# Optimization experiments

Hardware: AMD Instinct MI355X
Metric: run time of the kernel (lower is better)

The kernel has to match this reference:

```python
import jax, jax.numpy as jnp
import numpy as np

H = 128
V = 50000
B = 128
T_C = 50
T_I = 32
T_Q = 32
EPISODES = 3


def gru_cell(x, h, Wih, Whh, bih, bhh):
    # torch GRUCell math
    gi = x @ Wih.T + bih
    gh = h @ Whh.T + bhh
    ir, iz, inn = jnp.split(gi, 3, axis=-1)
    hr, hz, hn = jnp.split(gh, 3, axis=-1)
    r = jax.nn.sigmoid(ir + hr)
    z = jax.nn.sigmoid(iz + hz)
    n = jnp.tanh(inn + r * hn)
    return (1.0 - z) * n + z * h


def gru_outputs(x, Wih, Whh, bih, bhh):
    # x: (N, T, H) -> hidden at every step, (N, T, H)
    h0 = jnp.zeros((x.shape[0], x.shape[2]), x.dtype)
    def step(h, xt):
        h2 = gru_cell(xt, h, Wih, Whh, bih, bhh)
        return h2, h2
    _, ys = jax.lax.scan(step, h0, jnp.swapaxes(x, 0, 1))
    return jnp.swapaxes(ys, 0, 1)


def setup_inputs():
    key = jax.random.key(0)
    ks = iter(jax.random.split(key, 48))
    s = 0.05
    def mat(shape):
        return (jax.random.normal(next(ks), shape) * s).astype(jnp.float32)
    def gru_p(in_dim):
        return mat((3 * H, in_dim)), mat((3 * H, H)), mat((3 * H,)), mat((3 * H,))
    embed = mat((V, H)).at[0].set(0.0)  # padding_idx=0
    ig_Wih, ig_Whh, ig_bih, ig_bhh = gru_p(H)
    qg_Wih, qg_Whh, qg_bih, qg_bhh = gru_p(H)
    at_Wih, at_Whh, at_bih, at_bhh = gru_p(H)
    me_Wih, me_Whh, me_bih, me_bhh = gru_p(H)
    an_Wih, an_Whh, an_bih, an_bhh = gru_p(2 * H)
    gate_W1 = mat((H, 4 * H)); gate_b1 = mat((H,))
    gate_W2 = mat((1, H)); gate_b2 = mat((1,))
    fc_W = mat((V, H)); fc_b = jnp.zeros((V,), jnp.float32)
    facts = jax.random.randint(next(ks), (B, T_C, T_I), 0, V)
    fact_masks = jnp.zeros((B, T_C, T_I), jnp.int32)  # 0 == real token
    questions = jax.random.randint(next(ks), (B, T_Q), 0, V)
    question_masks = jnp.zeros((B, T_Q), jnp.int32)
    return dict(facts=facts, fact_masks=fact_masks, questions=questions,
                question_masks=question_masks, num_decode=8, embed=embed,
                ig_Wih=ig_Wih, ig_Whh=ig_Whh, ig_bih=ig_bih, ig_bhh=ig_bhh,
                qg_Wih=qg_Wih, qg_Whh=qg_Whh, qg_bih=qg_bih, qg_bhh=qg_bhh,
                at_Wih=at_Wih, at_Whh=at_Whh, at_bih=at_bih, at_bhh=at_bhh,
                me_Wih=me_Wih, me_Whh=me_Whh, me_bih=me_bih, me_bhh=me_bhh,
                an_Wih=an_Wih, an_Whh=an_Whh, an_bih=an_bih, an_bhh=an_bhh,
                gate_W1=gate_W1, gate_b1=gate_b1, gate_W2=gate_W2, gate_b2=gate_b2,
                fc_W=fc_W, fc_b=fc_b)


def reference(facts, fact_masks, questions, question_masks, num_decode, embed,
              ig_Wih, ig_Whh, ig_bih, ig_bhh,
              qg_Wih, qg_Whh, qg_bih, qg_bhh,
              at_Wih, at_Whh, at_bih, at_bhh,
              me_Wih, me_Whh, me_bih, me_bhh,
              an_Wih, an_Whh, an_bih, an_bhh,
              gate_W1, gate_b1, gate_W2, gate_b2, fc_W, fc_b):
    Bv, Tc, Ti = facts.shape
    Hd = embed.shape[1]

    # ---- fact encoding: one batched GRU over all B*T_C facts ----
    f = facts.reshape(Bv * Tc, Ti)
    emb = embed[f]                                            # (B*Tc, Ti, H)
    outs = gru_outputs(emb, ig_Wih, ig_Whh, ig_bih, ig_bhh)
    flen = jnp.sum(fact_masks.reshape(Bv * Tc, Ti) == 0, axis=-1)
    enc_f = jnp.take_along_axis(outs, (flen - 1)[:, None, None], axis=1)[:, 0]
    enc_f = enc_f.reshape(Bv, Tc, Hd)                         # (B, T_C, H)

    # ---- question encoding ----
    qouts = gru_outputs(embed[questions], qg_Wih, qg_Whh, qg_bih, qg_bhh)
    qlen = jnp.sum(question_masks == 0, axis=-1)
    q = jnp.take_along_axis(qouts, (qlen - 1)[:, None, None], axis=1)[:, 0]  # (B, H)

    # ---- episodic memory ----
    memory = q
    facts_t = jnp.swapaxes(enc_f, 0, 1)                       # (T_C, B, H)
    for _ in range(EPISODES):
        m = memory
        def ep_step(h, ft):
            z = jnp.concatenate([ft * q, ft * m, jnp.abs(ft - q), jnp.abs(ft - m)], axis=-1)
            g = jax.nn.sigmoid(jnp.tanh(z @ gate_W1.T + gate_b1) @ gate_W2.T + gate_b2)  # (B,1)
            h2 = gru_cell(ft, h, at_Wih, at_Whh, at_bih, at_bhh)
            return g * h2 + (1.0 - g) * h, None
        e, _ = jax.lax.scan(ep_step, jnp.zeros_like(memory), facts_t)
        memory = gru_cell(e, memory, me_Wih, me_Whh, me_bih, me_bhh)

    # ---- answer decoding (y_{t-1} stays the <s> embedding, as in the source) ----
    y0 = jnp.broadcast_to(embed[2], (Bv, Hd))                 # <s> token id = 2
    yq = jnp.concatenate([y0, q], axis=-1)                    # (B, 2H)
    def dec_step(h, _):
        h2 = gru_cell(yq, h, an_Wih, an_Whh, an_bih, an_bhh)
        return h2, jax.nn.log_softmax(h2 @ fc_W.T + fc_b, axis=-1)
    _, dec = jax.lax.scan(dec_step, memory, None, length=num_decode)  # (T, B, V)
    return jnp.swapaxes(dec, 0, 1).reshape(Bv * num_decode, -1)
```

## Files before the change

kernel.cpp:

```cpp
#include <hip/hip_runtime.h>
#include <math.h>

#define H   128
#define H3  384
#define TC  50
#define TI  32
#define TQ  32
#define NB  128
#define NF  (NB*TC)
#define EPISODES 3
#define LSLICE 25

typedef short  bf16x8 __attribute__((ext_vector_type(8)));
typedef short  bf16x4 __attribute__((ext_vector_type(4)));
typedef float  f32x4  __attribute__((ext_vector_type(4)));

__device__ __forceinline__ float dot4(float4 a, float4 b) {
  return a.x*b.x + a.y*b.y + a.z*b.z + a.w*b.w;
}
__device__ __forceinline__ float sigm(float x) { return 1.f/(1.f + __expf(-x)); }
__device__ __forceinline__ float tanh_f(float x) { return 1.f - 2.f/(1.f + __expf(2.f*x)); }
__device__ __forceinline__ float gru_comb(float ir, float iz, float inn,
                                          float hr, float hz, float hn, float h) {
  float r = sigm(ir + hr);
  float z = sigm(iz + hz);
  float n = tanh_f(inn + r*hn);
  return (1.f - z)*n + z*h;
}
__device__ __forceinline__ short f2bf(float x) {
  union { float f; unsigned u; } v; v.f = x;
  unsigned r = v.u + 0x7fffu + ((v.u >> 16) & 1u);
  return (short)(r >> 16);
}
__device__ __forceinline__ float bf2f(short s) {
  union { unsigned u; float f; } v; v.u = ((unsigned)(unsigned short)s) << 16;
  return v.f;
}
__device__ __forceinline__ bf16x8 pack8(float4 lo, float4 hi) {
  bf16x8 o;
  o[0]=f2bf(lo.x); o[1]=f2bf(lo.y); o[2]=f2bf(lo.z); o[3]=f2bf(lo.w);
  o[4]=f2bf(hi.x); o[5]=f2bf(hi.y); o[6]=f2bf(hi.z); o[7]=f2bf(hi.w);
  return o;
}

// ... 68 lines not shown
  int q = lane >> 4, l15 = lane & 15;
  f32x4 acc[8];
  #pragma unroll
  for (int nt = 0; nt < 8; ++nt) { acc[nt][0]=0.f; acc[nt][1]=0.f; acc[nt][2]=0.f; acc[nt][3]=0.f; }
  int mrow = wave*16 + l15;
  #pragma unroll
  for (int kf = 0; kf < 4; ++kf) {
    bf16x8 a = *(bf16x8*)&As[mrow][q*8 + kf*32];
    #pragma unroll
    for (int nt = 0; nt < 8; ++nt) {
      bf16x8 b = *(bf16x8*)&Bs[nt*16 + l15][q*8 + kf*32];
      acc[nt] = __builtin_amdgcn_mfma_f32_16x16x32_bf16(a, b, acc[nt], 0, 0, 0);
    }
  }
  __syncthreads();
  #pragma unroll
  for (int nt = 0; nt < 8; ++nt) {
    int col = nt*16 + l15;
    float bv = bias[bn*128 + col];
    #pragma unroll
    for (int reg = 0; reg < 4; ++reg)
      Bs[wave*16 + q*4 + reg][col] = f2bf(acc[nt][reg] + bv);
  }
  __syncthreads();
  #pragma unroll
  for (int i = 0; i < 4; ++i) {
    int idx = tid + i*256;
    int r = idx >> 4, e = (idx & 15)*8;
    int gr = bm*64 + r;
    if (gr < M) *(bf16x8*)(C + (size_t)gr*N + bn*128 + e) = *(bf16x8*)&Bs[r][e];
  }
}

__global__ __launch_bounds__(256) void k_copy(const float* __restrict__ src,
    float* __restrict__ dst, int n)
{
  int i = blockIdx.x*256 + threadIdx.x;
  if (i < n) dst[i] = src[i];
}

#define GI_STR 392
__global__ __launch_bounds__(512) void k_recgru2(
    const short* __restrict__ GI, const int* __restrict__ toks,
    const int* __restrict__ masks,
    const float* __restrict__ Whh, const float* __restrict__ bhh,
    float* __restrict__ enc_out, int steps)
{
  __shared__ __align__(16) short hsb[2][16][136];
  __shared__ __align__(16) short gib[2][16][GI_STR];
  __shared__ int ltoks[16*TI];
  __shared__ int enc_step_s[16];
  int tid = threadIdx.x;
  int lane = tid & 63, wave = tid >> 6;
  int q = lane >> 4, l15 = lane & 15;
  int seq0 = blockIdx.x * 16;

  for (int i = tid; i < 2*16*136; i += 512) ((short*)hsb)[i] = 0;
  if (toks) for (int i = tid; i < 16*steps; i += 512)
    ltoks[i] = toks[(size_t)seq0*steps + i];
  if (tid < 16) {
    int fl = 0;
    for (int i = 0; i < steps; ++i) fl += (masks[(size_t)(seq0+tid)*steps + i] == 0);
    int et = fl - 1; if (et < 0) et = 0; if (et >= steps) et = steps-1;
    enc_step_s[tid] = et;
  }
  bf16x8 wfrag[3][4];
  #pragma unroll
  for (int i = 0; i < 3; ++i) {
    int n = 16*wave + 128*i + l15;
    const float* wr = Whh + (size_t)n*H + q*8;
    #pragma unroll
    for (int kf = 0; kf < 4; ++kf)
      wfrag[i][kf] = pack8(*(const float4*)(wr + kf*32), *(const float4*)(wr + kf*32 + 4));
  }
  int c = 16*wave + l15;
  float bh0 = bhh[c], bh1 = bhh[c+H], bh2 = bhh[c+2*H];
  int ch0 = tid, ch1 = tid + 512;
  int r0 = ch0/48, o0 = ch0 - r0*48;
  int r1 = ch1/48, o1 = ch1 - r1*48;
  __syncthreads();
  int es[4];
  #pragma unroll
  for (int reg = 0; reg < 4; ++reg) es[reg] = enc_step_s[q*4 + reg];

  {
    size_t row0 = toks ? (size_t)ltoks[r0*steps] : ((size_t)(seq0 + r0)*steps);
    *(bf16x8*)&gib[0][r0][o0*8] = *((const bf16x8*)(GI + row0*H3) + o0);
    if (tid < 256) {
      size_t row1 = toks ? (size_t)ltoks[r1*steps] : ((size_t)(seq0 + r1)*steps);
      *(bf16x8*)&gib[0][r1][o1*8] = *((const bf16x8*)(GI + row1*H3) + o1);
    }
  }
  __syncthreads();

  float hreg[4] = {0.f, 0.f, 0.f, 0.f};
  for (int t = 0; t < steps; ++t) {
    bf16x8 pf0, pf1;
    bool havepf = (t + 1 < steps);
    if (havepf) {
      size_t row0 = toks ? (size_t)ltoks[r0*steps + t + 1]
                         : ((size_t)(seq0 + r0)*steps + t + 1);
      pf0 = *((const bf16x8*)(GI + row0*H3) + o0);
      if (tid < 256) {
        size_t row1 = toks ? (size_t)ltoks[r1*steps + t + 1]
                           : ((size_t)(seq0 + r1)*steps + t + 1);
        pf1 = *((const bf16x8*)(GI + row1*H3) + o1);
      }
    }
    f32x4 acc[3];
    #pragma unroll
    for (int i = 0; i < 3; ++i) { acc[i][0]=0.f; acc[i][1]=0.f; acc[i][2]=0.f; acc[i][3]=0.f; }
    #pragma unroll
    for (int kf = 0; kf < 4; ++kf) {
      bf16x8 a = *(bf16x8*)&hsb[t & 1][l15][kf*32 + q*8];
      #pragma unroll
      for (int i = 0; i < 3; ++i)
        acc[i] = __builtin_amdgcn_mfma_f32_16x16x32_bf16(a, wfrag[i][kf], acc[i], 0, 0, 0);
    }
    #pragma unroll
    for (int reg = 0; reg < 4; ++reg) {
      int row = q*4 + reg;
      float gr = bf2f(gib[t & 1][row][c]);
      float gz = bf2f(gib[t & 1][row][c + 128]);
      float gn = bf2f(gib[t & 1][row][c + 256]);
      float hnew = gru_comb(gr, gz, gn,
                            acc[0][reg] + bh0, acc[1][reg] + bh1, acc[2][reg] + bh2,
                            hreg[reg]);
      hreg[reg] = hnew;
      hsb[(t + 1) & 1][row][c] = f2bf(hnew);
      if (t == es[reg]) enc_out[(size_t)(seq0 + row)*H + c] = hnew;
    }
    if (havepf) {
      *(bf16x8*)&gib[(t + 1) & 1][r0][o0*8] = pf0;
      if (tid < 256) *(bf16x8*)&gib[(t + 1) & 1][r1][o1*8] = pf1;
    }
    __syncthreads();
  }
}

__global__ __launch_bounds__(512) void k_recgru3(
    const short* __restrict__ GI, const int* __restrict__ toks,
    const int* __restrict__ masks,
    const float* __restrict__ Whh, const float* __restrict__ bhh,
    float* __restrict__ enc_out, int steps)
{
  __shared__ __align__(16) short hsb[2][32][136];
  __shared__ __align__(16) short gib[2][25][GI_STR];
  __shared__ int ltoks[25*TI];
  __shared__ int enc_step_s[25];
  int tid = threadIdx.x;
  int lane = tid & 63, wave = tid >> 6;
  int q = lane >> 4, l15 = lane & 15;
  int seq0 = blockIdx.x * 25;

  for (int i = tid; i < 2*32*136; i += 512) ((short*)hsb)[i] = 0;
  for (int i = tid; i < 25*steps; i += 512)
    ltoks[i] = toks[(size_t)seq0*steps + i];
  if (tid < 25) {
    int fl = 0;
    for (int i = 0; i < steps; ++i) fl += (masks[(size_t)(seq0+tid)*steps + i] == 0);
    int et = fl - 1; if (et < 0) et = 0; if (et >= steps) et = steps-1;
    enc_step_s[tid] = et;
  }
  bf16x8 wfrag[3][4];
  #pragma unroll
  for (int i = 0; i < 3; ++i) {
    int n = 16*wave + 128*i + l15;
    const float* wr = Whh + (size_t)n*H + q*8;
    #pragma unroll
    for (int kf = 0; kf < 4; ++kf)
      wfrag[i][kf] = pack8(*(const float4*)(wr + kf*32), *(const float4*)(wr + kf*32 + 4));
  }
  int c = 16*wave + l15;
  float bh0 = bhh[c], bh1 = bhh[c+H], bh2 = bhh[c+2*H];
  int ch0 = tid, ch1 = tid + 512, ch2 = tid + 1024;
  int r0 = ch0/48, o0 = ch0 - r0*48;
  int r1 = ch1/48, o1 = ch1 - r1*48;
  int r2 = ch2/48, o2 = ch2 - r2*48;
  __syncthreads();
  int es0[4], es1[4];
  #pragma unroll
  for (int reg = 0; reg < 4; ++reg) {
    es0[reg] = enc_step_s[q*4 + reg];
    int row2 = 16 + q*4 + reg;
    es1[reg] = (row2 < 25) ? enc_step_s[row2] : -9;
  }
  {
    *(bf16x8*)&gib[0][r0][o0*8] = *((const bf16x8*)(GI + (size_t)ltoks[r0*steps]*H3) + o0);
    *(bf16x8*)&gib[0][r1][o1*8] = *((const bf16x8*)(GI + (size_t)ltoks[r1*steps]*H3) + o1);
    if (tid < 176)
      *(bf16x8*)&gib[0][r2][o2*8] = *((const bf16x8*)(GI + (size_t)ltoks[r2*steps]*H3) + o2);
  }
  __syncthreads();

  float h0[4] = {0.f,0.f,0.f,0.f}, h1[4] = {0.f,0.f,0.f,0.f};
  for (int t = 0; t < steps; ++t) {
    bf16x8 pf0, pf1, pf2;
    bool havepf = (t + 1 < steps);
    if (havepf) {
      pf0 = *((const bf16x8*)(GI + (size_t)ltoks[r0*steps + t + 1]*H3) + o0);
      pf1 = *((const bf16x8*)(GI + (size_t)ltoks[r1*steps + t + 1]*H3) + o1);
      if (tid < 176)
        pf2 = *((const bf16x8*)(GI + (size_t)ltoks[r2*steps + t + 1]*H3) + o2);
    }
    f32x4 acc0[3], acc1[3];
    acc0[0] = (f32x4){bh0,bh0,bh0,bh0};
    acc0[1] = (f32x4){bh1,bh1,bh1,bh1};
    acc0[2] = (f32x4){bh2,bh2,bh2,bh2};
    acc1[0] = acc0[0]; acc1[1] = acc0[1]; acc1[2] = acc0[2];
    #pragma unroll
    for (int kf = 0; kf < 4; ++kf) {
      bf16x8 a0 = *(bf16x8*)&hsb[t & 1][l15][kf*32 + q*8];
      bf16x8 a1 = *(bf16x8*)&hsb[t & 1][16 + l15][kf*32 + q*8];
      #pragma unroll
      for (int i = 0; i < 3; ++i) {
        acc0[i] = __builtin_amdgcn_mfma_f32_16x16x32_bf16(a0, wfrag[i][kf], acc0[i], 0, 0, 0);
        acc1[i] = __builtin_amdgcn_mfma_f32_16x16x32_bf16(a1, wfrag[i][kf], acc1[i], 0, 0, 0);
      }
    }
    #pragma unroll
    for (int reg = 0; reg < 4; ++reg) {
      int row = q*4 + reg;
      float gr = bf2f(gib[t & 1][row][c]);
      float gz = bf2f(gib[t & 1][row][c + 128]);
      float gn = bf2f(gib[t & 1][row][c + 256]);
      float hnew = gru_comb(gr, gz, gn, acc0[0][reg], acc0[1][reg], acc0[2][reg], h0[reg]);
      h0[reg] = hnew;
      hsb[(t + 1) & 1][row][c] = f2bf(hnew);
      if (t == es0[reg]) enc_out[(size_t)(seq0 + row)*H + c] = hnew;
      int row2 = row + 16;
      if (row2 < 25) {
        float gr2 = bf2f(gib[t & 1][row2][c]);
        float gz2 = bf2f(gib[t & 1][row2][c + 128]);
        float gn2 = bf2f(gib[t & 1][row2][c + 256]);
        float hnew2 = gru_comb(gr2, gz2, gn2, acc1[0][reg], acc1[1][reg], acc1[2][reg], h1[reg]);
        h1[reg] = hnew2;
        hsb[(t + 1) & 1][row2][c] = f2bf(hnew2);
        if (t == es1[reg]) enc_out[(size_t)(seq0 + row2)*H + c] = hnew2;
      }
    }
    if (havepf) {
      *(bf16x8*)&gib[(t + 1) & 1][r0][o0*8] = pf0;
      *(bf16x8*)&gib[(t + 1) & 1][r1][o1*8] = pf1;
      if (tid < 176) *(bf16x8*)&gib[(t + 1) & 1][r2][o2*8] = pf2;
    }
    __syncthreads();
  }
}

__global__ __launch_bounds__(128) void k_gatepre(const float* __restrict__ encf,
    const float* __restrict__ qv, const float* __restrict__ W1,
    const float* __restrict__ b1, float* __restrict__ U1)
{
  __shared__ float us[16][H], vs[16][H];
  int tid = threadIdx.x;
  int nt0 = blockIdx.x * 16;
  for (int i = tid; i < 16*H; i += 128) {
    int r = i >> 7, k = i & 127;
    int nt = nt0 + r, n = nt / TC;
    float f = encf[(size_t)nt*H + k];
    float q = qv[(size_t)n*H + k];
    us[r][k] = f*q;
    vs[r][k] = fabsf(f - q);
  }
  __syncthreads();
  int c = tid;
  float acc[16] = {};
  const float* wa = W1 + (size_t)c*(4*H);
  const float* wc = wa + 2*H;
  for (int kk = 0; kk < H; kk += 16) {
    float4 a0 = *(const float4*)(wa + kk);
    float4 a1 = *(const float4*)(wa + kk + 4);
    float4 a2 = *(const float4*)(wa + kk + 8);
    float4 a3 = *(const float4*)(wa + kk + 12);
    float4 c0 = *(const float4*)(wc + kk);
    float4 c1 = *(const float4*)(wc + kk + 4);
    float4 c2 = *(const float4*)(wc + kk + 8);
    float4 c3 = *(const float4*)(wc + kk + 12);
    #pragma unroll
    for (int r = 0; r < 16; ++r) {
      const float* up = &us[r][kk];
      const float* vp = &vs[r][kk];
      acc[r] += dot4(*(const float4*)up,     a0) + dot4(*(const float4*)(up+4), a1)
              + dot4(*(const float4*)(up+8), a2) + dot4(*(const float4*)(up+12),a3)
              + dot4(*(const float4*)vp,     c0) + dot4(*(const float4*)(vp+4), c1)
              + dot4(*(const float4*)(vp+8), c2) + dot4(*(const float4*)(vp+12),c3);
    }
  }
  float bb = b1[c];
  #pragma unroll
  for (int r = 0; r < 16; ++r) U1[(size_t)(nt0 + r)*H + c] = acc[r] + bb;
}

__global__ __launch_bounds__(128) void k_gate(const float* __restrict__ encf,
    const float* __restrict__ mem, const float* __restrict__ W1,
    const float* __restrict__ W2, const float* __restrict__ b2,
    const float* __restrict__ U1, float* __restrict__ gate)
{
  __shared__ float us[16][H], vs[16][H], hid[16][H], parts[16][8];
  int tid = threadIdx.x;
  int nt0 = blockIdx.x * 16;
  for (int i = tid; i < 16*H; i += 128) {
    int r = i >> 7, k = i & 127;
    int nt = nt0 + r, n = nt / TC;
    float f = encf[(size_t)nt*H + k];
    float m = mem[(size_t)n*H + k];
    us[r][k] = f*m;
    vs[r][k] = fabsf(f - m);
  }
  __syncthreads();
  int c = tid;
  float acc[16];
  #pragma unroll
  for (int r = 0; r < 16; ++r) acc[r] = U1[(size_t)(nt0 + r)*H + c];
  const float* wb = W1 + (size_t)c*(4*H) + H;
  const float* wd = W1 + (size_t)c*(4*H) + 3*H;
  for (int kk = 0; kk < H; kk += 16) {
    float4 a0 = *(const float4*)(wb + kk);
    float4 a1 = *(const float4*)(wb + kk + 4);
    float4 a2 = *(const float4*)(wb + kk + 8);
    float4 a3 = *(const float4*)(wb + kk + 12);
    float4 c0 = *(const float4*)(wd + kk);
    float4 c1 = *(const float4*)(wd + kk + 4);
    float4 c2 = *(const float4*)(wd + kk + 8);
// ... 196 lines not shown
    gis[0][tid] = b + se + sq0;
    gis[1][tid] = b + se + sq1;
  }
  const float* whp = an_Whh + (size_t)tid*H;
  float bh = an_bhh[tid];
  for (int t = 0; t < ND; ++t) {
    float a0 = 0.f, a1 = 0.f;
    for (int kk = 0; kk < H; kk += 16) {
      float4 w0 = *(const float4*)(whp + kk);
      float4 w1 = *(const float4*)(whp + kk + 4);
      float4 w2 = *(const float4*)(whp + kk + 8);
      float4 w3 = *(const float4*)(whp + kk + 12);
      const float* h0p = &hs[0][kk];
      const float* h1p = &hs[1][kk];
      a0 += dot4(*(const float4*)h0p,     w0) + dot4(*(const float4*)(h0p+4), w1)
          + dot4(*(const float4*)(h0p+8), w2) + dot4(*(const float4*)(h0p+12),w3);
      a1 += dot4(*(const float4*)h1p,     w0) + dot4(*(const float4*)(h1p+4), w1)
          + dot4(*(const float4*)(h1p+8), w2) + dot4(*(const float4*)(h1p+12),w3);
    }
    ghs[0][tid] = a0 + bh;
    ghs[1][tid] = a1 + bh;
    __syncthreads();
    if (tid < 256) {
      int r = tid >> 7, c = tid & 127;
      float h2 = gru_comb(gis[r][c], gis[r][c+H], gis[r][c+2*H],
                          ghs[r][c], ghs[r][c+H], ghs[r][c+2*H], hs[r][c]);
      hs[r][c] = h2;
      h2d16[((size_t)(n0 + r)*ND + t)*H + c] = f2bf(h2);
    }
    __syncthreads();
  }
}

__global__ __launch_bounds__(256) void k_lpass1(const short* __restrict__ A16,
    const short* __restrict__ B16, const float* __restrict__ bias,
    float2* __restrict__ partials, int M, int N)
{
  __shared__ __align__(16) short As[64][136];
  __shared__ __align__(16) short Bs[128][136];
  int tid = threadIdx.x;
  int lane = tid & 63, wave = tid >> 6;
  int q = lane >> 4, l15 = lane & 15;
  int bm = blockIdx.x, sl = blockIdx.y;
  #pragma unroll
  for (int i = 0; i < 4; ++i) {
    int ch = tid + i*256;
    int r = ch >> 4, e = (ch & 15)*8;
    int gr = bm*64 + r; if (gr > M-1) gr = M-1;
    *(bf16x8*)&As[r][e] = *(const bf16x8*)(A16 + (size_t)gr*H + e);
  }
  int mrow = wave*16 + l15;
  float m[4] = {-3.4e38f, -3.4e38f, -3.4e38f, -3.4e38f};
  float s[4] = {0.f, 0.f, 0.f, 0.f};
  for (int chn = 0; chn < 16; ++chn) {
    int c0 = sl*2048 + chn*128;
    #pragma unroll
    for (int i = 0; i < 8; ++i) {
      int ch = tid + i*256;
      int r = ch >> 4, e = (ch & 15)*8;
      int gn = c0 + r; if (gn > N-1) gn = N-1;
      *(bf16x8*)&Bs[r][e] = *(const bf16x8*)(B16 + (size_t)gn*H + e);
    }
    __syncthreads();
    f32x4 acc[8];
    #pragma unroll
    for (int nt = 0; nt < 8; ++nt) { acc[nt][0]=0.f; acc[nt][1]=0.f; acc[nt][2]=0.f; acc[nt][3]=0.f; }
    #pragma unroll
    for (int kf = 0; kf < 4; ++kf) {
      bf16x8 a = *(bf16x8*)&As[mrow][q*8 + kf*32];
      #pragma unroll
      for (int nt = 0; nt < 8; ++nt) {
        bf16x8 b = *(bf16x8*)&Bs[nt*16 + l15][q*8 + kf*32];
        acc[nt] = __builtin_amdgcn_mfma_f32_16x16x32_bf16(a, b, acc[nt], 0, 0, 0);
      }
    }
    __syncthreads();
    float bv[8];
    #pragma unroll
    for (int nt = 0; nt < 8; ++nt) {
      int col = c0 + nt*16 + l15;
      bv[nt] = (col < N) ? bias[col] : 0.f;
    }
    #pragma unroll
    for (int reg = 0; reg < 4; ++reg) {
      float xs[8], cm = -3.4e38f;
      #pragma unroll
      for (int nt = 0; nt < 8; ++nt) {
        int col = c0 + nt*16 + l15;
        float x = (col < N) ? (acc[nt][reg] + bv[nt]) : -3.4e38f;
        xs[nt] = x; cm = fmaxf(cm, x);
      }
      float nm = fmaxf(m[reg], cm);
      float ss = s[reg] * __expf(m[reg] - nm);
      #pragma unroll
      for (int nt = 0; nt < 8; ++nt) ss += __expf(xs[nt] - nm);
      m[reg] = nm; s[reg] = ss;
    }
  }
  #pragma unroll
  for (int off = 1; off < 16; off <<= 1) {
    #pragma unroll
    for (int reg = 0; reg < 4; ++reg) {
      float mo = __shfl_xor(m[reg], off);
      float so = __shfl_xor(s[reg], off);
      float nm = fmaxf(m[reg], mo);
      s[reg] = s[reg]*__expf(m[reg] - nm) + so*__expf(mo - nm);
      m[reg] = nm;
    }
  }
  if (l15 == 0) {
    #pragma unroll
    for (int reg = 0; reg < 4; ++reg) {
      int row = bm*64 + wave*16 + q*4 + reg;
      if (row < M) partials[(size_t)row*LSLICE + sl] = make_float2(m[reg], s[reg]);
    }
  }
}

__global__ __launch_bounds__(256) void k_lse(const float2* __restrict__ partials,
                                             float* __restrict__ lse, int M)
{
  int row = blockIdx.x*256 + threadIdx.x;
  if (row >= M) return;
  float m = -3.4e38f, s = 0.f;
  for (int i = 0; i < LSLICE; ++i) {
    float2 p = partials[(size_t)row*LSLICE + i];
    float nm = fmaxf(m, p.x);
    s = s*__expf(m - nm) + p.y*__expf(p.x - nm);
    m = nm;
  }
  lse[row] = m + logf(s);
}

__global__ __launch_bounds__(256) void k_lpass2(const short* __restrict__ A16,
    const short* __restrict__ B16, const float* __restrict__ B32,
    const float* __restrict__ bias, const float* __restrict__ lse,
    float* __restrict__ C, int M, int N, int bm_off)
{
  __shared__ __align__(16) short As[64][136];
  __shared__ __align__(16) short Bs[128][136];
  int tid = threadIdx.x;
  int lane = tid & 63, wave = tid >> 6;
  int q = lane >> 4, l15 = lane & 15;
  int bm = blockIdx.x + bm_off, bn = blockIdx.y;
  #pragma unroll
  for (int i = 0; i < 4; ++i) {
    int ch = tid + i*256;
    int r = ch >> 4, e = (ch & 15)*8;
    int gr = bm*64 + r; if (gr > M-1) gr = M-1;
    *(bf16x8*)&As[r][e] = *(const bf16x8*)(A16 + (size_t)gr*H + e);
  }
  if (B16) {
    #pragma unroll
    for (int i = 0; i < 8; ++i) {
      int ch = tid + i*256;
      int r = ch >> 4, e = (ch & 15)*8;
      int gn = bn*128 + r; if (gn > N-1) gn = N-1;
      *(bf16x8*)&Bs[r][e] = *(const bf16x8*)(B16 + (size_t)gn*H + e);
    }
  } else {
    #pragma unroll
    for (int i = 0; i < 8; ++i) {
      int ch = tid + i*256;
      int r = ch >> 4, e = (ch & 15)*8;
// ... 56 lines not shown
  const int*   facts     = (const int*)  d_in[0];
  const int*   fmask     = (const int*)  d_in[1];
  const int*   questions = (const int*)  d_in[2];
  const int*   qmask     = (const int*)  d_in[3];
  const float* embed     = (const float*)d_in[5];
  const float* ig_Wih    = (const float*)d_in[6];
  const float* ig_Whh    = (const float*)d_in[7];
  const float* ig_bih    = (const float*)d_in[8];
  const float* ig_bhh    = (const float*)d_in[9];
  const float* qg_Wih    = (const float*)d_in[10];
  const float* qg_Whh    = (const float*)d_in[11];
  const float* qg_bih    = (const float*)d_in[12];
  const float* qg_bhh    = (const float*)d_in[13];
  const float* at_Wih    = (const float*)d_in[14];
  const float* at_Whh    = (const float*)d_in[15];
  const float* at_bih    = (const float*)d_in[16];
  const float* at_bhh    = (const float*)d_in[17];
  const float* me_Wih    = (const float*)d_in[18];
  const float* me_Whh    = (const float*)d_in[19];
  const float* me_bih    = (const float*)d_in[20];
  const float* me_bhh    = (const float*)d_in[21];
  const float* an_Wih    = (const float*)d_in[22];
  const float* an_Whh    = (const float*)d_in[23];
  const float* an_bih    = (const float*)d_in[24];
  const float* an_bhh    = (const float*)d_in[25];
  const float* gate_W1   = (const float*)d_in[26];
  const float* gate_b1   = (const float*)d_in[27];
  const float* gate_W2   = (const float*)d_in[28];
  const float* gate_b2   = (const float*)d_in[29];
  const float* fc_W      = (const float*)d_in[30];
  const float* fc_b      = (const float*)d_in[31];
  (void)n_in; (void)ws_size;

  const int V  = in_sizes[5] / H;
  const int ND = out_size / (NB * V);
  const int M  = NB * ND;
  const int BMT = M / 64;

  float* OUT = (float*)d_out;
  size_t oP     = 0;
  size_t oEMB16 = (size_t)V*192;
  size_t oEMBQ  = oEMB16 + (size_t)V*64;
  size_t oQGI   = oEMBQ + (size_t)NB*TQ*64;
  size_t oGIAT  = oQGI  + (size_t)NB*TQ*192;
  size_t oU1    = oGIAT + (size_t)NF*192;
  size_t oGATE  = oU1   + (size_t)NF*H;
  size_t oW16   = oGATE + NF;
  short* Psh    = (short*)(OUT + oP);
  short* EMB16  = (short*)(OUT + oEMB16);
  short* EMBQ16 = (short*)(OUT + oEMBQ);
  short* QGIsh  = (short*)(OUT + oQGI);
  short* GIATsh = (short*)(OUT + oGIAT);
  float* U1b    = OUT + oU1;
  float* GATE   = OUT + oGATE;
  short* igW16  = (short*)(OUT + oW16);
  short* qgW16  = igW16 + (size_t)H3*H;
  short* atW16  = qgW16 + (size_t)H3*H;
  short* FCW16  = (short*)(OUT + (size_t)(M - 64)*V);

  float* encf  = (float*)d_ws;
  float* qvec  = encf + (size_t)NF*H;
  float* mem   = qvec + (size_t)NB*H;
  short* H2D16 = (short*)(mem + (size_t)NB*H);
  float* lse   = (float*)(H2D16 + (size_t)M*H);
  float2* partials = (float2*)(lse + M);

  k_cvtall<<<2632, 256, 0, stream>>>(embed, EMB16, fc_W, FCW16,
                                     ig_Wih, qg_Wih, at_Wih, igW16, V*H);
  k_mgemmX<<<dim3((V+63)/64, H3/128), 256, 0, stream>>>(EMB16, nullptr, igW16, ig_bih, Psh, V, H3);
  k_gather16<<<NB*TQ/8, 256, 0, stream>>>(EMB16, questions, EMBQ16);
  k_mgemmX<<<dim3(NB*TQ/64, H3/128), 256, 0, stream>>>(EMBQ16, nullptr, qgW16, qg_bih, QGIsh, NB*TQ, H3);
  k_recgru3<<<NF/25, 512, 0, stream>>>(Psh, facts, fmask, ig_Whh, ig_bhh, encf, TI);
  k_recgru2<<<NB/16, 512, 0, stream>>>(QGIsh, nullptr, qmask, qg_Whh, qg_bhh, qvec, TQ);
  k_mgemmX<<<dim3(NF/64, H3/128), 256, 0, stream>>>(nullptr, encf, atW16, at_bih, GIATsh, NF, H3);
  k_gatepre<<<NF/16, 128, 0, stream>>>(encf, qvec, gate_W1, gate_b1, U1b);
  k_copy<<<(NB*H+255)/256, 256, 0, stream>>>(qvec, mem, NB*H);
  for (int e = 0; e < EPISODES; ++e) {
    k_gate<<<NF/16, 128, 0, stream>>>(encf, mem, gate_W1, gate_W2, gate_b2, U1b, GATE);
    k_episode2<<<NB/16, 512, 0, stream>>>(GIATsh, GATE, at_Whh, at_bhh,
                                          me_Wih, me_Whh, me_bih, me_bhh, mem);
  }
  k_decode<<<NB/2, 384, 0, stream>>>(embed, qvec, mem, an_Wih, an_Whh, an_bih, an_bhh,
                                     H2D16, ND);
  k_lpass1<<<dim3(BMT, LSLICE), 256, 0, stream>>>(H2D16, FCW16, fc_b, partials, M, V);
  k_lse<<<(M+255)/256, 256, 0, stream>>>(partials, lse, M);
  k_lpass2<<<dim3(BMT-1, (V+127)/128), 256, 0, stream>>>(H2D16, FCW16, nullptr, fc_b, lse,
                                                         OUT, M, V, 0);
  k_lpass2<<<dim3(1, (V+127)/128), 256, 0, stream>>>(H2D16, nullptr, fc_W, fc_b, lse,
                                                     OUT, M, V, BMT-1);
}
```

Measured before the change: 978.7 us.

## Fuse fact input projection into GRU, fuse first gate, restructure logit passes

The fact encoder no longer precomputes input projections for the whole vocabulary. It gathers bf16 embeddings per step and computes the input gates with MFMA inside the recurrent kernel, which removes the V x 384 GEMM and its scratch buffer. The first episode's gate is computed inside the gate-precompute kernel, and the question GRU writes the initial memory directly, so a copy kernel and one gate launch go away. The logit passes are now tiled by vocabulary column, with each block keeping its FC weight tile in LDS and looping over row tiles. This adds per-step MFMA work in the recurrence and finer-grained LSE partials.

New measurement: 1.076 ms. 1.1x slower.

```diff
diff --git a/kernel.cpp b/kernel.cpp
--- a/kernel.cpp
+++ b/kernel.cpp
@@ -9,7 +9,6 @@
 #define NB  128
 #define NF  (NB*TC)
 #define EPISODES 3
-#define LSLICE 25
 
 typedef short  bf16x8 __attribute__((ext_vector_type(8)));
 typedef short  bf16x4 __attribute__((ext_vector_type(4)));
@@ -144,23 +143,14 @@
   }
 }
 
-__global__ __launch_bounds__(256) void k_copy(const float* __restrict__ src,
-    float* __restrict__ dst, int n)
-{
-  int i = blockIdx.x*256 + threadIdx.x;
-  if (i < n) dst[i] = src[i];
-}
-
 #define GI_STR 392
 __global__ __launch_bounds__(512) void k_recgru2(
-    const short* __restrict__ GI, const int* __restrict__ toks,
-    const int* __restrict__ masks,
+    const short* __restrict__ GI, const int* __restrict__ masks,
     const float* __restrict__ Whh, const float* __restrict__ bhh,
-    float* __restrict__ enc_out, int steps)
+    float* __restrict__ enc_out, float* __restrict__ mem_out, int steps)
 {
   __shared__ __align__(16) short hsb[2][16][136];
   __shared__ __align__(16) short gib[2][16][GI_STR];
-  __shared__ int ltoks[16*TI];
   __shared__ int enc_step_s[16];
   int tid = threadIdx.x;
   int lane = tid & 63, wave = tid >> 6;
@@ -168,8 +158,6 @@
   int seq0 = blockIdx.x * 16;
 
   for (int i = tid; i < 2*16*136; i += 512) ((short*)hsb)[i] = 0;
-  if (toks) for (int i = tid; i < 16*steps; i += 512)
-    ltoks[i] = toks[(size_t)seq0*steps + i];
   if (tid < 16) {
     int fl = 0;
     for (int i = 0; i < steps; ++i) fl += (masks[(size_t)(seq0+tid)*steps + i] == 0);
@@ -196,10 +184,10 @@
   for (int reg = 0; reg < 4; ++reg) es[reg] = enc_step_s[q*4 + reg];
 
   {
-    size_t row0 = toks ? (size_t)ltoks[r0*steps] : ((size_t)(seq0 + r0)*steps);
+    size_t row0 = (size_t)(seq0 + r0)*steps;
     *(bf16x8*)&gib[0][r0][o0*8] = *((const bf16x8*)(GI + row0*H3) + o0);
     if (tid < 256) {
-      size_t row1 = toks ? (size_t)ltoks[r1*steps] : ((size_t)(seq0 + r1)*steps);
+      size_t row1 = (size_t)(seq0 + r1)*steps;
       *(bf16x8*)&gib[0][r1][o1*8] = *((const bf16x8*)(GI + row1*H3) + o1);
     }
   }
@@ -210,12 +198,10 @@
     bf16x8 pf0, pf1;
     bool havepf = (t + 1 < steps);
     if (havepf) {
-      size_t row0 = toks ? (size_t)ltoks[r0*steps + t + 1]
-                         : ((size_t)(seq0 + r0)*steps + t + 1);
+      size_t row0 = (size_t)(seq0 + r0)*steps + t + 1;
       pf0 = *((const bf16x8*)(GI + row0*H3) + o0);
       if (tid < 256) {
-        size_t row1 = toks ? (size_t)ltoks[r1*steps + t + 1]
-                           : ((size_t)(seq0 + r1)*steps + t + 1);
+        size_t row1 = (size_t)(seq0 + r1)*steps + t + 1;
         pf1 = *((const bf16x8*)(GI + row1*H3) + o1);
       }
     }
@@ -240,7 +226,10 @@
                             hreg[reg]);
       hreg[reg] = hnew;
       hsb[(t + 1) & 1][row][c] = f2bf(hnew);
-      if (t == es[reg]) enc_out[(size_t)(seq0 + row)*H + c] = hnew;
+      if (t == es[reg]) {
+        enc_out[(size_t)(seq0 + row)*H + c] = hnew;
+        if (mem_out) mem_out[(size_t)(seq0 + row)*H + c] = hnew;
+      }
     }
     if (havepf) {
       *(bf16x8*)&gib[(t + 1) & 1][r0][o0*8] = pf0;
@@ -250,14 +239,14 @@
   }
 }
 
-__global__ __launch_bounds__(512) void k_recgru3(
-    const short* __restrict__ GI, const int* __restrict__ toks,
-    const int* __restrict__ masks,
-    const float* __restrict__ Whh, const float* __restrict__ bhh,
-    float* __restrict__ enc_out, int steps)
+__global__ __launch_bounds__(512) void k_facts(
+    const short* __restrict__ EMB16, const short* __restrict__ WI,
+    const int* __restrict__ toks, const int* __restrict__ masks,
+    const float* __restrict__ Whh, const float* __restrict__ bih,
+    const float* __restrict__ bhh, float* __restrict__ enc_out, int steps)
 {
   __shared__ __align__(16) short hsb[2][32][136];
-  __shared__ __align__(16) short gib[2][25][GI_STR];
+  __shared__ __align__(16) short esb[2][32][136];
   __shared__ int ltoks[25*TI];
   __shared__ int enc_step_s[25];
   int tid = threadIdx.x;
@@ -265,7 +254,7 @@
   int q = lane >> 4, l15 = lane & 15;
   int seq0 = blockIdx.x * 25;
 
-  for (int i = tid; i < 2*32*136; i += 512) ((short*)hsb)[i] = 0;
+  for (int i = tid; i < 2*32*136; i += 512) { ((short*)hsb)[i] = 0; ((short*)esb)[i] = 0; }
   for (int i = tid; i < 25*steps; i += 512)
     ltoks[i] = toks[(size_t)seq0*steps + i];
   if (tid < 25) {
@@ -274,21 +263,22 @@
     int et = fl - 1; if (et < 0) et = 0; if (et >= steps) et = steps-1;
     enc_step_s[tid] = et;
   }
-  bf16x8 wfrag[3][4];
+  bf16x8 wI[3][4], wH[3][4];
   #pragma unroll
   for (int i = 0; i < 3; ++i) {
     int n = 16*wave + 128*i + l15;
-    const float* wr = Whh + (size_t)n*H + q*8;
-    #pragma unroll
-    for (int kf = 0; kf < 4; ++kf)
-      wfrag[i][kf] = pack8(*(const float4*)(wr + kf*32), *(const float4*)(wr + kf*32 + 4));
+    #pragma unroll
+    for (int kf = 0; kf < 4; ++kf) {
+      wI[i][kf] = *(const bf16x8*)(WI + (size_t)n*H + kf*32 + q*8);
+      const float* wr = Whh + (size_t)n*H + kf*32 + q*8;
+      wH[i][kf] = pack8(*(const float4*)wr, *(const float4*)(wr + 4));
+    }
   }
   int c = 16*wave + l15;
+  float bi0 = bih[c], bi1 = bih[c+H], bi2 = bih[c+2*H];
   float bh0 = bhh[c], bh1 = bhh[c+H], bh2 = bhh[c+2*H];
-  int ch0 = tid, ch1 = tid + 512, ch2 = tid + 1024;
-  int r0 = ch0/48, o0 = ch0 - r0*48;
-  int r1 = ch1/48, o1 = ch1 - r1*48;
-  int r2 = ch2/48, o2 = ch2 - r2*48;
+  int er = tid >> 4, eo = tid & 15;
+  bool act = er < 25;
   __syncthreads();
   int es0[4], es1[4];
   #pragma unroll
@@ -297,74 +287,85 @@
     int row2 = 16 + q*4 + reg;
     es1[reg] = (row2 < 25) ? enc_step_s[row2] : -9;
   }
-  {
-    *(bf16x8*)&gib[0][r0][o0*8] = *((const bf16x8*)(GI + (size_t)ltoks[r0*steps]*H3) + o0);
-    *(bf16x8*)&gib[0][r1][o1*8] = *((const bf16x8*)(GI + (size_t)ltoks[r1*steps]*H3) + o1);
-    if (tid < 176)
-      *(bf16x8*)&gib[0][r2][o2*8] = *((const bf16x8*)(GI + (size_t)ltoks[r2*steps]*H3) + o2);
+  if (act) {
+    int tk = ltoks[er*steps];
+    *(bf16x8*)&esb[0][er][eo*8] = *((const bf16x8*)(EMB16 + (size_t)tk*H) + eo);
   }
   __syncthreads();
 
   float h0[4] = {0.f,0.f,0.f,0.f}, h1[4] = {0.f,0.f,0.f,0.f};
   for (int t = 0; t < steps; ++t) {
-    bf16x8 pf0, pf1, pf2;
-    bool havepf = (t + 1 < steps);
+    int cur = t & 1, nxt = cur ^ 1;
+    bf16x8 pf;
+    bool havepf = (t + 1 < steps) && act;
     if (havepf) {
-      pf0 = *((const bf16x8*)(GI + (size_t)ltoks[r0*steps + t + 1]*H3) + o0);
-      pf1 = *((const bf16x8*)(GI + (size_t)ltoks[r1*steps + t + 1]*H3) + o1);
-      if (tid < 176)
-        pf2 = *((const bf16x8*)(GI + (size_t)ltoks[r2*steps + t + 1]*H3) + o2);
-    }
-    f32x4 acc0[3], acc1[3];
-    acc0[0] = (f32x4){bh0,bh0,bh0,bh0};
-    acc0[1] = (f32x4){bh1,bh1,bh1,bh1};
-    acc0[2] = (f32x4){bh2,bh2,bh2,bh2};
-    acc1[0] = acc0[0]; acc1[1] = acc0[1]; acc1[2] = acc0[2];
+      int tk = ltoks[er*steps + t + 1];
+      pf = *((const bf16x8*)(EMB16 + (size_t)tk*H) + eo);
+    }
+    f32x4 gi[3], gh[3];
+    gi[0] = (f32x4){bi0,bi0,bi0,bi0};
+    gi[1] = (f32x4){bi1,bi1,bi1,bi1};
+    gi[2] = (f32x4){bi2,bi2,bi2,bi2};
+    gh[0] = (f32x4){bh0,bh0,bh0,bh0};
+    gh[1] = (f32x4){bh1,bh1,bh1,bh1};
+    gh[2] = (f32x4){bh2,bh2,bh2,bh2};
     #pragma unroll
     for (int kf = 0; kf < 4; ++kf) {
-      bf16x8 a0 = *(bf16x8*)&hsb[t & 1][l15][kf*32 + q*8];
-      bf16x8 a1 = *(bf16x8*)&hsb[t & 1][16 + l15][kf*32 + q*8];
+      bf16x8 ae = *(bf16x8*)&esb[cur][l15][kf*32 + q*8];
+      bf16x8 ah = *(bf16x8*)&hsb[cur][l15][kf*32 + q*8];
       #pragma unroll
       for (int i = 0; i < 3; ++i) {
-        acc0[i] = __builtin_amdgcn_mfma_f32_16x16x32_bf16(a0, wfrag[i][kf], acc0[i], 0, 0, 0);
-        acc1[i] = __builtin_amdgcn_mfma_f32_16x16x32_bf16(a1, wfrag[i][kf], acc1[i], 0, 0, 0);
+        gi[i] = __builtin_amdgcn_mfma_f32_16x16x32_bf16(ae, wI[i][kf], gi[i], 0, 0, 0);
+        gh[i] = __builtin_amdgcn_mfma_f32_16x16x32_bf16(ah, wH[i][kf], gh[i], 0, 0, 0);
       }
     }
     #pragma unroll
     for (int reg = 0; reg < 4; ++reg) {
       int row = q*4 + reg;
-      float gr = bf2f(gib[t & 1][row][c]);
-      float gz = bf2f(gib[t & 1][row][c + 128]);
-      float gn = bf2f(gib[t & 1][row][c + 256]);
-      float hnew = gru_comb(gr, gz, gn, acc0[0][reg], acc0[1][reg], acc0[2][reg], h0[reg]);
+      float hnew = gru_comb(gi[0][reg], gi[1][reg], gi[2][reg],
+                            gh[0][reg], gh[1][reg], gh[2][reg], h0[reg]);
       h0[reg] = hnew;
-      hsb[(t + 1) & 1][row][c] = f2bf(hnew);
+      hsb[nxt][row][c] = f2bf(hnew);
       if (t == es0[reg]) enc_out[(size_t)(seq0 + row)*H + c] = hnew;
-      int row2 = row + 16;
+    }
+    gi[0] = (f32x4){bi0,bi0,bi0,bi0};
+    gi[1] = (f32x4){bi1,bi1,bi1,bi1};
+    gi[2] = (f32x4){bi2,bi2,bi2,bi2};
+    gh[0] = (f32x4){bh0,bh0,bh0,bh0};
+    gh[1] = (f32x4){bh1,bh1,bh1,bh1};
+    gh[2] = (f32x4){bh2,bh2,bh2,bh2};
+    #pragma unroll
+    for (int kf = 0; kf < 4; ++kf) {
+      bf16x8 ae = *(bf16x8*)&esb[cur][16 + l15][kf*32 + q*8];
+      bf16x8 ah = *(bf16x8*)&hsb[cur][16 + l15][kf*32 + q*8];
+      #pragma unroll
+      for (int i = 0; i < 3; ++i) {
+        gi[i] = __builtin_amdgcn_mfma_f32_16x16x32_bf16(ae, wI[i][kf], gi[i], 0, 0, 0);
+        gh[i] = __builtin_amdgcn_mfma_f32_16x16x32_bf16(ah, wH[i][kf], gh[i], 0, 0, 0);
+      }
+    }
+    #pragma unroll
+    for (int reg = 0; reg < 4; ++reg) {
+      int row2 = 16 + q*4 + reg;
       if (row2 < 25) {
-        float gr2 = bf2f(gib[t & 1][row2][c]);
-        float gz2 = bf2f(gib[t & 1][row2][c + 128]);
-        float gn2 = bf2f(gib[t & 1][row2][c + 256]);
-        float hnew2 = gru_comb(gr2, gz2, gn2, acc1[0][reg], acc1[1][reg], acc1[2][reg], h1[reg]);
-        h1[reg] = hnew2;
-        hsb[(t + 1) & 1][row2][c] = f2bf(hnew2);
-        if (t == es1[reg]) enc_out[(size_t)(seq0 + row2)*H + c] = hnew2;
-      }
-    }
-    if (havepf) {
-      *(bf16x8*)&gib[(t + 1) & 1][r0][o0*8] = pf0;
-      *(bf16x8*)&gib[(t + 1) & 1][r1][o1*8] = pf1;
-      if (tid < 176) *(bf16x8*)&gib[(t + 1) & 1][r2][o2*8] = pf2;
-    }
+        float hnew = gru_comb(gi[0][reg], gi[1][reg], gi[2][reg],
+                              gh[0][reg], gh[1][reg], gh[2][reg], h1[reg]);
+        h1[reg] = hnew;
+        hsb[nxt][row2][c] = f2bf(hnew);
+        if (t == es1[reg]) enc_out[(size_t)(seq0 + row2)*H + c] = hnew;
+      }
+    }
+    if (havepf) *(bf16x8*)&esb[nxt][er][eo*8] = pf;
     __syncthreads();
   }
 }
 
-__global__ __launch_bounds__(128) void k_gatepre(const float* __restrict__ encf,
+__global__ __launch_bounds__(128) void k_gatepre2(const float* __restrict__ encf,
     const float* __restrict__ qv, const float* __restrict__ W1,
-    const float* __restrict__ b1, float* __restrict__ U1)
-{
-  __shared__ float us[16][H], vs[16][H];
+    const float* __restrict__ b1, const float* __restrict__ W2,
+    const float* __restrict__ b2, float* __restrict__ U1, float* __restrict__ gate)
+{
+  __shared__ float us[16][H], vs[16][H], hid[16][H], parts[16][8];
   int tid = threadIdx.x;
   int nt0 = blockIdx.x * 16;
   for (int i = tid; i < 16*H; i += 128) {
@@ -378,30 +379,74 @@
   __syncthreads();
   int c = tid;
   float acc[16] = {};
-  const float* wa = W1 + (size_t)c*(4*H);
-  const float* wc = wa + 2*H;
-  for (int kk = 0; kk < H; kk += 16) {
-    float4 a0 = *(const float4*)(wa + kk);
-    float4 a1 = *(const float4*)(wa + kk + 4);
-    float4 a2 = *(const float4*)(wa + kk + 8);
-    float4 a3 = *(const float4*)(wa + kk + 12);
-    float4 c0 = *(const float4*)(wc + kk);
-    float4 c1 = *(const float4*)(wc + kk + 4);
-    float4 c2 = *(const float4*)(wc + kk + 8);
-    float4 c3 = *(const float4*)(wc + kk + 12);
-    #pragma unroll
-    for (int r = 0; r < 16; ++r) {
-      const float* up = &us[r][kk];
-      const float* vp = &vs[r][kk];
-      acc[r] += dot4(*(const float4*)up,     a0) + dot4(*(const float4*)(up+4), a1)
-              + dot4(*(const float4*)(up+8), a2) + dot4(*(const float4*)(up+12),a3)
-              + dot4(*(const float4*)vp,     c0) + dot4(*(const float4*)(vp+4), c1)
-              + dot4(*(const float4*)(vp+8), c2) + dot4(*(const float4*)(vp+12),c3);
+  {
+    const float* wa = W1 + (size_t)c*(4*H);
+    const float* wc = wa + 2*H;
+    for (int kk = 0; kk < H; kk += 16) {
+      float4 a0 = *(const float4*)(wa + kk);
+      float4 a1 = *(const float4*)(wa + kk + 4);
+      float4 a2 = *(const float4*)(wa + kk + 8);
+      float4 a3 = *(const float4*)(wa + kk + 12);
+      float4 c0 = *(const float4*)(wc + kk);
+      float4 c1 = *(const float4*)(wc + kk + 4);
+      float4 c2 = *(const float4*)(wc + kk + 8);
+      float4 c3 = *(const float4*)(wc + kk + 12);
+      #pragma unroll
+      for (int r = 0; r < 16; ++r) {
+        const float* up = &us[r][kk];
+        const float* vp = &vs[r][kk];
+        acc[r] += dot4(*(const float4*)up,     a0) + dot4(*(const float4*)(up+4), a1)
+                + dot4(*(const float4*)(up+8), a2) + dot4(*(const float4*)(up+12),a3)
+                + dot4(*(const float4*)vp,     c0) + dot4(*(const float4*)(vp+4), c1)
+                + dot4(*(const float4*)(vp+8), c2) + dot4(*(const float4*)(vp+12),c3);
+      }
+    }
+  }
+  float accm[16] = {};
+  {
+    const float* wb = W1 + (size_t)c*(4*H) + H;
+    const float* wd = W1 + (size_t)c*(4*H) + 3*H;
+    for (int kk = 0; kk < H; kk += 16) {
+      float4 a0 = *(const float4*)(wb + kk);
+      float4 a1 = *(const float4*)(wb + kk + 4);
+      float4 a2 = *(const float4*)(wb + kk + 8);
+      float4 a3 = *(const float4*)(wb + kk + 12);
+      float4 c0 = *(const float4*)(wd + kk);
+      float4 c1 = *(const float4*)(wd + kk + 4);
+      float4 c2 = *(const float4*)(wd + kk + 8);
+      float4 c3 = *(const float4*)(wd + kk + 12);
+      #pragma unroll
+      for (int r = 0; r < 16; ++r) {
+        const float* up = &us[r][kk];
+        const float* vp = &vs[r][kk];
+        accm[r] += dot4(*(const float4*)up,     a0) + dot4(*(const float4*)(up+4), a1)
+                 + dot4(*(const float4*)(up+8), a2) + dot4(*(const float4*)(up+12),a3)
+                 + dot4(*(const float4*)vp,     c0) + dot4(*(const float4*)(vp+4), c1)
+                 + dot4(*(const float4*)(vp+8), c2) + dot4(*(const float4*)(vp+12),c3);
+      }
     }
   }
   float bb = b1[c];
   #pragma unroll
-  for (int r = 0; r < 16; ++r) U1[(size_t)(nt0 + r)*H + c] = acc[r] + bb;
+  for (int r = 0; r < 16; ++r) {
+    float u = acc[r] + bb;
+    U1[(size_t)(nt0 + r)*H + c] = u;
+    hid[r][c] = tanh_f(u + accm[r]);
+  }
+  __syncthreads();
+  {
+    int r = tid >> 3, i = tid & 7;
+    float p = 0.f;
+    for (int k = i*16; k < i*16 + 16; ++k) p += hid[r][k]*W2[k];
+    parts[r][i] = p;
+  }
+  __syncthreads();
+  if (tid < 16) {
+    float s = b2[0];
+    #pragma unroll
+    for (int i = 0; i < 8; ++i) s += parts[tid][i];
+    gate[nt0 + tid] = sigm(s);
+  }
 }
 
 __global__ __launch_bounds__(128) void k_gate(const float* __restrict__ encf,
@@ -664,34 +709,37 @@
   }
 }
 
-__global__ __launch_bounds__(256) void k_lpass1(const short* __restrict__ A16,
+__global__ __launch_bounds__(256) void k_lpass1p(const short* __restrict__ A16,
     const short* __restrict__ B16, const float* __restrict__ bias,
-    float2* __restrict__ partials, int M, int N)
+    float2* __restrict__ partials, int M, int N, int NSL)
 {
   __shared__ __align__(16) short As[64][136];
   __shared__ __align__(16) short Bs[128][136];
   int tid = threadIdx.x;
   int lane = tid & 63, wave = tid >> 6;
   int q = lane >> 4, l15 = lane & 15;
-  int bm = blockIdx.x, sl = blockIdx.y;
-  #pragma unroll
-  for (int i = 0; i < 4; ++i) {
+  int bn = blockIdx.x;
+  #pragma unroll
+  for (int i = 0; i < 8; ++i) {
     int ch = tid + i*256;
     int r = ch >> 4, e = (ch & 15)*8;
-    int gr = bm*64 + r; if (gr > M-1) gr = M-1;
-    *(bf16x8*)&As[r][e] = *(const bf16x8*)(A16 + (size_t)gr*H + e);
+    int gn = bn*128 + r; if (gn > N-1) gn = N-1;
+    *(bf16x8*)&Bs[r][e] = *(const bf16x8*)(B16 + (size_t)gn*H + e);
+  }
+  float bv[8];
+  #pragma unroll
+  for (int nt = 0; nt < 8; ++nt) {
+    int col = bn*128 + nt*16 + l15;
+    bv[nt] = (col < N) ? bias[col] : 0.f;
   }
   int mrow = wave*16 + l15;
-  float m[4] = {-3.4e38f, -3.4e38f, -3.4e38f, -3.4e38f};
-  float s[4] = {0.f, 0.f, 0.f, 0.f};
-  for (int chn = 0; chn < 16; ++chn) {
-    int c0 = sl*2048 + chn*128;
-    #pragma unroll
-    for (int i = 0; i < 8; ++i) {
+  for (int rt = 0; rt < 16; ++rt) {
+    __syncthreads();
+    #pragma unroll
+    for (int i = 0; i < 4; ++i) {
       int ch = tid + i*256;
       int r = ch >> 4, e = (ch & 15)*8;
-      int gn = c0 + r; if (gn > N-1) gn = N-1;
-      *(bf16x8*)&Bs[r][e] = *(const bf16x8*)(B16 + (size_t)gn*H + e);
+      *(bf16x8*)&As[r][e] = *(const bf16x8*)(A16 + (size_t)(rt*64 + r)*H + e);
     }
     __syncthreads();
     f32x4 acc[8];
@@ -706,62 +754,109 @@
         acc[nt] = __builtin_amdgcn_mfma_f32_16x16x32_bf16(a, b, acc[nt], 0, 0, 0);
       }
     }
-    __syncthreads();
-    float bv[8];
-    #pragma unroll
-    for (int nt = 0; nt < 8; ++nt) {
-      int col = c0 + nt*16 + l15;
-      bv[nt] = (col < N) ? bias[col] : 0.f;
-    }
     #pragma unroll
     for (int reg = 0; reg < 4; ++reg) {
       float xs[8], cm = -3.4e38f;
       #pragma unroll
       for (int nt = 0; nt < 8; ++nt) {
-        int col = c0 + nt*16 + l15;
+        int col = bn*128 + nt*16 + l15;
         float x = (col < N) ? (acc[nt][reg] + bv[nt]) : -3.4e38f;
         xs[nt] = x; cm = fmaxf(cm, x);
       }
-      float nm = fmaxf(m[reg], cm);
-      float ss = s[reg] * __expf(m[reg] - nm);
-      #pragma unroll
-      for (int nt = 0; nt < 8; ++nt) ss += __expf(xs[nt] - nm);
-      m[reg] = nm; s[reg] = ss;
-    }
-  }
-  #pragma unroll
-  for (int off = 1; off < 16; off <<= 1) {
-    #pragma unroll
-    for (int reg = 0; reg < 4; ++reg) {
-      float mo = __shfl_xor(m[reg], off);
-      float so = __shfl_xor(s[reg], off);
-      float nm = fmaxf(m[reg], mo);
-      s[reg] = s[reg]*__expf(m[reg] - nm) + so*__expf(mo - nm);
-      m[reg] = nm;
-    }
-  }
-  if (l15 == 0) {
-    #pragma unroll
-    for (int reg = 0; reg < 4; ++reg) {
-      int row = bm*64 + wave*16 + q*4 + reg;
-      if (row < M) partials[(size_t)row*LSLICE + sl] = make_float2(m[reg], s[reg]);
+      float ss = 0.f;
+      #pragma unroll
+      for (int nt = 0; nt < 8; ++nt) ss += __expf(xs[nt] - cm);
+      float m = cm, s = ss;
+      #pragma unroll
+      for (int off = 1; off < 16; off <<= 1) {
+        float mo = __shfl_xor(m, off);
+        float so = __shfl_xor(s, off);
+        float nm = fmaxf(m, mo);
+        s = s*__expf(m - nm) + so*__expf(mo - nm);
+        m = nm;
+      }
+      if (l15 == 0) {
+        int row = rt*64 + wave*16 + q*4 + reg;
+        partials[(size_t)row*NSL + bn] = make_float2(m, s);
+      }
     }
   }
 }
 
 __global__ __launch_bounds__(256) void k_lse(const float2* __restrict__ partials,
-                                             float* __restrict__ lse, int M)
+                                             float* __restrict__ lse, int M, int NSL)
 {
   int row = blockIdx.x*256 + threadIdx.x;
   if (row >= M) return;
   float m = -3.4e38f, s = 0.f;
-  for (int i = 0; i < LSLICE; ++i) {
-    float2 p = partials[(size_t)row*LSLICE + i];
+  for (int i = 0; i < NSL; ++i) {
+    float2 p = partials[(size_t)row*NSL + i];
     float nm = fmaxf(m, p.x);
     s = s*__expf(m - nm) + p.y*__expf(p.x - nm);
     m = nm;
   }
   lse[row] = m + logf(s);
+}
+
+__global__ __launch_bounds__(256) void k_lpass2p(const short* __restrict__ A16,
+    const short* __restrict__ B16, const float* __restrict__ bias,
+    const float* __restrict__ lse, float* __restrict__ C, int M, int N, int NT)
+{
+  __shared__ __align__(16) short As[64][136];
+  __shared__ __align__(16) short Bs[128][136];
+  __shared__ float lss[960];
+  int tid = threadIdx.x;
+  int lane = tid & 63, wave = tid >> 6;
+  int q = lane >> 4, l15 = lane & 15;
+  int bn = blockIdx.x;
+  #pragma unroll
+  for (int i = 0; i < 8; ++i) {
+    int ch = tid + i*256;
+    int r = ch >> 4, e = (ch & 15)*8;
+    int gn = bn*128 + r; if (gn > N-1) gn = N-1;
+    *(bf16x8*)&Bs[r][e] = *(const bf16x8*)(B16 + (size_t)gn*H + e);
+  }
+  for (int i = tid; i < NT*64; i += 256) lss[i] = lse[i];
+  float bv[8];
+  #pragma unroll
+  for (int nt = 0; nt < 8; ++nt) {
+    int col = bn*128 + nt*16 + l15;
+    bv[nt] = (col < N) ? bias[col] : 0.f;
+  }
+  int mrow = wave*16 + l15;
+  for (int rt = 0; rt < NT; ++rt) {
+    __syncthreads();
+    #pragma unroll
+    for (int i = 0; i < 4; ++i) {
+      int ch = tid + i*256;
+      int r = ch >> 4, e = (ch & 15)*8;
+      *(bf16x8*)&As[r][e] = *(const bf16x8*)(A16 + (size_t)(rt*64 + r)*H + e);
+    }
+    __syncthreads();
+    f32x4 acc[8];
+    #pragma unroll
+    for (int nt = 0; nt < 8; ++nt) { acc[nt][0]=0.f; acc[nt][1]=0.f; acc[nt][2]=0.f; acc[nt][3]=0.f; }
+    #pragma unroll
+    for (int kf = 0; kf < 4; ++kf) {
+      bf16x8 a = *(bf16x8*)&As[mrow][q*8 + kf*32];
+      #pragma unroll
+      for (int nt = 0; nt < 8; ++nt) {
+        bf16x8 b = *(bf16x8*)&Bs[nt*16 + l15][q*8 + kf*32];
+        acc[nt] = __builtin_amdgcn_mfma_f32_16x16x32_bf16(a, b, acc[nt], 0, 0, 0);
+      }
+    }
+    #pragma unroll
+    for (int nt = 0; nt < 8; ++nt) {
+      int gcol = bn*128 + nt*16 + l15;
+      if (gcol < N) {
+        #pragma unroll
+        for (int reg = 0; reg < 4; ++reg) {
+          int row = rt*64 + wave*16 + q*4 + reg;
+          C[(size_t)row*N + gcol] = acc[nt][reg] + bv[nt] - lss[row];
+        }
+      }
+    }
+  }
 }
 
 __global__ __launch_bounds__(256) void k_lpass2(const short* __restrict__ A16,
@@ -884,21 +979,21 @@
   const float* fc_b      = (const float*)d_in[31];
   (void)n_in; (void)ws_size;
 
-  const int V  = in_sizes[5] / H;
-  const int ND = out_size / (NB * V);
-  const int M  = NB * ND;
-  const int BMT = M / 64;
+  const int V   = in_sizes[5] / H;
+  const int ND  = out_size / (NB * V);
+  const int M   = NB * ND;
+  const int NSL = (V + 127) / 128;
 
   float* OUT = (float*)d_out;
-  size_t oP     = 0;
-  size_t oEMB16 = (size_t)V*192;
+  size_t oPART  = 0;
+  size_t oEMB16 = oPART + (size_t)M*NSL*2;
   size_t oEMBQ  = oEMB16 + (size_t)V*64;
   size_t oQGI   = oEMBQ + (size_t)NB*TQ*64;
   size_t oGIAT  = oQGI  + (size_t)NB*TQ*192;
   size_t oU1    = oGIAT + (size_t)NF*192;
   size_t oGATE  = oU1   + (size_t)NF*H;
   size_t oW16   = oGATE + NF;
-  short* Psh    = (short*)(OUT + oP);
+  float2* partials = (float2*)(OUT + oPART);
   short* EMB16  = (short*)(OUT + oEMB16);
   short* EMBQ16 = (short*)(OUT + oEMBQ);
   short* QGIsh  = (short*)(OUT + oQGI);
@@ -915,29 +1010,27 @@
   float* mem   = qvec + (size_t)NB*H;
   short* H2D16 = (short*)(mem + (size_t)NB*H);
   float* lse   = (float*)(H2D16 + (size_t)M*H);
-  float2* partials = (float2*)(lse + M);
 
   k_cvtall<<<2632, 256, 0, stream>>>(embed, EMB16, fc_W, FCW16,
                                      ig_Wih, qg_Wih, at_Wih, igW16, V*H);
-  k_mgemmX<<<dim3((V+63)/64, H3/128), 256, 0, stream>>>(EMB16, nullptr, igW16, ig_bih, Psh, V, H3);
   k_gather16<<<NB*TQ/8, 256, 0, stream>>>(EMB16, questions, EMBQ16);
   k_mgemmX<<<dim3(NB*TQ/64, H3/128), 256, 0, stream>>>(EMBQ16, nullptr, qgW16, qg_bih, QGIsh, NB*TQ, H3);
-  k_recgru3<<<NF/25, 512, 0, stream>>>(Psh, facts, fmask, ig_Whh, ig_bhh, encf, TI);
-  k_recgru2<<<NB/16, 512, 0, stream>>>(QGIsh, nullptr, qmask, qg_Whh, qg_bhh, qvec, TQ);
+  k_facts<<<NF/25, 512, 0, stream>>>(EMB16, igW16, facts, fmask, ig_Whh, ig_bih, ig_bhh, encf, TI);
+  k_recgru2<<<NB/16, 512, 0, stream>>>(QGIsh, qmask, qg_Whh, qg_bhh, qvec, mem, TQ);
   k_mgemmX<<<dim3(NF/64, H3/128), 256, 0, stream>>>(nullptr, encf, atW16, at_bih, GIATsh, NF, H3);
-  k_gatepre<<<NF/16, 128, 0, stream>>>(encf, qvec, gate_W1, gate_b1, U1b);
-  k_copy<<<(NB*H+255)/256, 256, 0, stream>>>(qvec, mem, NB*H);
-  for (int e = 0; e < EPISODES; ++e) {
+  k_gatepre2<<<NF/16, 128, 0, stream>>>(encf, qvec, gate_W1, gate_b1, gate_W2, gate_b2, U1b, GATE);
+  k_episode2<<<NB/16, 512, 0, stream>>>(GIATsh, GATE, at_Whh, at_bhh,
+                                        me_Wih, me_Whh, me_bih, me_bhh, mem);
+  for (int e = 1; e < EPISODES; ++e) {
     k_gate<<<NF/16, 128, 0, stream>>>(encf, mem, gate_W1, gate_W2, gate_b2, U1b, GATE);
     k_episode2<<<NB/16, 512, 0, stream>>>(GIATsh, GATE, at_Whh, at_bhh,
                                           me_Wih, me_Whh, me_bih, me_bhh, mem);
   }
   k_decode<<<NB/2, 384, 0, stream>>>(embed, qvec, mem, an_Wih, an_Whh, an_bih, an_bhh,
                                      H2D16, ND);
-  k_lpass1<<<dim3(BMT, LSLICE), 256, 0, stream>>>(H2D16, FCW16, fc_b, partials, M, V);
-  k_lse<<<(M+255)/256, 256, 0, stream>>>(partials, lse, M);
-  k_lpass2<<<dim3(BMT-1, (V+127)/128), 256, 0, stream>>>(H2D16, FCW16, nullptr, fc_b, lse,
-                                                         OUT, M, V, 0);
-  k_lpass2<<<dim3(1, (V+127)/128), 256, 0, stream>>>(H2D16, nullptr, fc_W, fc_b, lse,
-                                                     OUT, M, V, BMT-1);
-}
+  k_lpass1p<<<NSL, 256, 0, stream>>>(H2D16, FCW16, fc_b, partials, M, V, NSL);
+  k_lse<<<(M+255)/256, 256, 0, stream>>>(partials, lse, M, NSL);
+  k_lpass2p<<<NSL, 256, 0, stream>>>(H2D16, FCW16, fc_b, lse, OUT, M, V, (M/64) - 1);
+  k_lpass2<<<dim3(1, NSL), 256, 0, stream>>>(H2D16, nullptr, fc_W, fc_b, lse,
+                                             OUT, M, V, (M/64) - 1);
+}
```
